# Optimization experiments

Hardware: AMD Instinct MI355X
Metric: run time of the kernel (lower is better)

The kernel has to match this reference:

```python
import jax, jax.numpy as jnp
import numpy as np

T, D, H, E = 8192, 1024, 512, 8
BLK = 32  # MXFP8 scaling block size along the contraction dim


def setup_inputs() -> dict:
    key = jax.random.key(0)
    k1, k2, k3, k4 = jax.random.split(key, 4)
    # qdata: values representable-ish in e4m3 (we use small normal floats)
    output_e4m3 = jax.random.normal(k1, (T, D), dtype=jnp.float32)
    # e8m0 scales are powers of two, one per 32-element block along dim
    output_scales_e8m0 = jnp.exp2(
        jax.random.randint(k2, (T, D // BLK), -2, 3).astype(jnp.float32)
    )
    # uniform token distribution across experts (tokens are expert-contiguous)
    num_tokens_per_expert = jnp.full((E,), T // E, dtype=jnp.int32)
    expert_padded_offsets = jnp.zeros((E,), dtype=jnp.int32)  # unused by forward body
    w13 = jax.random.normal(k3, (E, 2 * H, D), dtype=jnp.float32) * 0.02
    w2 = jax.random.normal(k4, (E, D, H), dtype=jnp.float32) * 0.02
    return {
        "output_e4m3": output_e4m3,
        "output_scales_e8m0": output_scales_e8m0,
        "num_tokens_per_expert": num_tokens_per_expert,
        "expert_padded_offsets": expert_padded_offsets,
        "w13": w13,
        "w2": w2,
    }


def reference(output_e4m3, output_scales_e8m0, num_tokens_per_expert,
              expert_padded_offsets, w13, w2):
    # Dequantize MXFP8: qdata * per-block e8m0 scale, blocks of 32 along dim.
    scales = jnp.repeat(output_scales_e8m0, BLK, axis=-1)  # [T, D]
    x = output_e4m3 * scales  # [T, D] high-precision reference activations
    # Grouped GEMM 1: tokens are expert-contiguous with uniform group sizes,
    # so the ragged grouped matmul reduces to a batched einsum per expert.
    tpe = T // E
    xg = x.reshape(E, tpe, D)                       # [E, tpe, D]
    h13 = jnp.einsum("etd,ehd->eth", xg, w13)       # [E, tpe, 2H]
    h1, h3 = h13[..., :H], h13[..., H:]
    h = jax.nn.silu(h1) * h3                        # fused SiLU-gate
    # Grouped GEMM 2
    out = jnp.einsum("eth,edh->etd", h, w2)         # [E, tpe, D]
    return out.reshape(T, D)
```

## Files before the change

kernel.cpp:

```cpp
#include <hip/hip_runtime.h>
#include <hip/hip_bf16.h>

#define T_TOK 8192
#define DDIM  1024
#define HDIM  512
#define NE    8
#define TPE   (T_TOK / NE)

typedef __attribute__((ext_vector_type(4))) float floatx4;
typedef __attribute__((ext_vector_type(8))) short bf16x8;

#define SBAR() __builtin_amdgcn_sched_barrier(0)

__device__ __forceinline__ unsigned short f2bf(float f) {
    union { float f; unsigned int u; } v;
    v.f = f;
    unsigned int u = v.u;
    unsigned int r = u + 0x7FFFu + ((u >> 16) & 1u);
    return (unsigned short)(r >> 16);
}

__device__ __forceinline__ unsigned int cvt_pk_bf16(float lo, float hi) {
    unsigned int r;
    asm("v_cvt_pk_bf16_f32 %0, %1, %2" : "=v"(r) : "v"(lo), "v"(hi));
    return r;
}

__device__ __forceinline__ void gld_lds16(const void* g, void* l) {
    __builtin_amdgcn_global_load_lds(
        (const __attribute__((address_space(1))) unsigned int*)g,
        (__attribute__((address_space(3))) unsigned int*)l, 16, 0, 0);
}

__global__ __launch_bounds__(256)
void convert_x_kernel(const float* __restrict__ X, const float* __restrict__ S,
                      unsigned short* __restrict__ Xb)
{
    const int NTX = (T_TOK * DDIM) / 4;
    const int stride = gridDim.x * blockDim.x;
    for (int i = blockIdx.x * blockDim.x + threadIdx.x; i < NTX; i += stride) {
        int row = i >> 8;
        int c4  = i & 255;
        float4 v = reinterpret_cast<const float4*>(X)[i];
        float sc = S[row * (DDIM / 32) + (c4 >> 3)];
        ushort4 b;
        b.x = f2bf(v.x * sc); b.y = f2bf(v.y * sc);
        b.z = f2bf(v.z * sc); b.w = f2bf(v.w * sc);
        reinterpret_cast<ushort4*>(Xb)[i] = b;
    }
}

__device__ __forceinline__ int xcd_swizzle_512(int raw) {
    return (raw & 7) * 64 + (raw >> 3);
}


__global__ __launch_bounds__(256, 2)
void gemm1_silu_kernel(const unsigned short* __restrict__ Xb,
                       const float* __restrict__ W13,
                       __hip_bfloat16* __restrict__ Hout)
{
    const int bid = xcd_swizzle_512(blockIdx.x);
    const int e  = bid >> 6;
    const int mt = (bid >> 3) & 7;
    const int nt = bid & 7;
    const int tok0 = e * TPE + mt * 128;
    const float* __restrict__ We = W13 + (size_t)e * (2 * HDIM) * DDIM;

    __shared__ __hip_bfloat16 sA[2][128][64];
    __shared__ __hip_bfloat16 sB[2][128][64];

    const int tid  = threadIdx.x;
    const int lane = tid & 63;
    const int wave = tid >> 6;
    const int wr = wave >> 1;
    const int wc = wave & 1;
    const int lr = lane & 15;
    const int sw0 = ((lane >> 4) ^ (lane & 7));

    floatx4 acc1[4][2] = {};
    floatx4 acc3[4][2] = {};

    const int srow0 = (tid >> 3);
    const int c8    = (tid & 7) * 8;
    const int dcol  = (tid & 7) * 8;
    const int gcol  = ((tid & 7) ^ (srow0 & 7)) * 8;
    const int swcol = gcol;

    float4 rB0[8], rB1[8];

    auto LOADB = [&](int kk, float4* rB) {
        const int k0 = kk * 64;
        #pragma unroll
        for (int j = 0; j < 4; ++j) {
            int row = srow0 + j * 32;
            int wrow = (j < 2) ? (nt * 64 + row)
                               : (HDIM + nt * 64 + (row - 64));
            const float* p = &We[(size_t)wrow * DDIM + k0 + c8];
            rB[2*j]   = *reinterpret_cast<const float4*>(p);
            rB[2*j+1] = *reinterpret_cast<const float4*>(p + 4);
        }
    };
    auto STAGEA = [&](int kk, int buf) {
        const int k0 = kk * 64;
        #pragma unroll
        for (int j = 0; j < 4; ++j) {
            int row = srow0 + j * 32;
            gld_lds16(&Xb[(size_t)(tok0 + row) * DDIM + k0 + gcol],
                      &sA[buf][row][dcol]);
        }
    };
    auto WRITEB = [&](int buf, const float4* rB) {
        #pragma unroll
        for (int j = 0; j < 4; ++j) {
            int row = srow0 + j * 32;
            uint4 w;
            w.x = cvt_pk_bf16(rB[2*j].x,   rB[2*j].y);
            w.y = cvt_pk_bf16(rB[2*j].z,   rB[2*j].w);
            w.z = cvt_pk_bf16(rB[2*j+1].x, rB[2*j+1].y);
            w.w = cvt_pk_bf16(rB[2*j+1].z, rB[2*j+1].w);
            *reinterpret_cast<uint4*>(&sB[buf][row][swcol]) = w;
        }
    };
    auto COMPUTE_KS = [&](int buf, int ks) {
        const int rc = (sw0 ^ (ks << 2)) << 3;
        bf16x8 a[4], b1[2], b3[2];
        #pragma unroll
        for (int m = 0; m < 4; ++m)
            a[m] = *reinterpret_cast<const bf16x8*>(&sA[buf][wr * 64 + m * 16 + lr][rc]);
        #pragma unroll
        for (int n = 0; n < 2; ++n) {
            b1[n] = *reinterpret_cast<const bf16x8*>(&sB[buf][wc * 32 + n * 16 + lr][rc]);
            b3[n] = *reinterpret_cast<const bf16x8*>(&sB[buf][64 + wc * 32 + n * 16 + lr][rc]);
        }
        #pragma unroll
        for (int m = 0; m < 4; ++m)
            #pragma unroll
            for (int n = 0; n < 2; ++n) {
                acc1[m][n] = __builtin_amdgcn_mfma_f32_16x16x32_bf16(a[m], b1[n], acc1[m][n], 0, 0, 0);
                acc3[m][n] = __builtin_amdgcn_mfma_f32_16x16x32_bf16(a[m], b3[n], acc3[m][n], 0, 0, 0);
            }
    };

    LOADB(0, rB0);  SBAR();
    STAGEA(0, 0);   SBAR();
    LOADB(1, rB1);  SBAR();
    asm volatile("s_waitcnt vmcnt(12)" ::: "memory");
    SBAR();
    WRITEB(0, rB0); SBAR();
    asm volatile("s_waitcnt vmcnt(8) lgkmcnt(0)" ::: "memory");
    SBAR();
    __builtin_amdgcn_s_barrier();

    for (int t = 0; t < DDIM / 64 - 2; t += 2) {
        STAGEA(t + 1, 1);   SBAR();
        LOADB(t + 2, rB0);  SBAR();
        COMPUTE_KS(0, 0);
        COMPUTE_KS(0, 1);
        asm volatile("s_waitcnt vmcnt(12)" ::: "memory");
        SBAR();
        WRITEB(1, rB1);     SBAR();
        asm volatile("s_waitcnt vmcnt(8) lgkmcnt(0)" ::: "memory");
        SBAR();
        __builtin_amdgcn_s_barrier();
        STAGEA(t + 2, 0);   SBAR();
        LOADB(t + 3, rB1);  SBAR();
        COMPUTE_KS(1, 0);
        COMPUTE_KS(1, 1);
        asm volatile("s_waitcnt vmcnt(12)" ::: "memory");
        SBAR();
        WRITEB(0, rB0);     SBAR();
        asm volatile("s_waitcnt vmcnt(8) lgkmcnt(0)" ::: "memory");
        SBAR();
        __builtin_amdgcn_s_barrier();
    }

    STAGEA(15, 1);    SBAR();
    COMPUTE_KS(0, 0);
    COMPUTE_KS(0, 1);
    asm volatile("s_waitcnt vmcnt(4)" ::: "memory");
    SBAR();
    WRITEB(1, rB1);   SBAR();
    asm volatile("s_waitcnt vmcnt(0) lgkmcnt(0)" ::: "memory");
    SBAR();
    __builtin_amdgcn_s_barrier();
    COMPUTE_KS(1, 0);
    COMPUTE_KS(1, 1);

    const int hcol0 = nt * 64 + wc * 32;
    #pragma unroll
    for (int m = 0; m < 4; ++m) {
        #pragma unroll
        for (int n = 0; n < 2; ++n) {
            #pragma unroll
            for (int i = 0; i < 4; ++i) {
                int row = tok0 + wr * 64 + m * 16 + (lane >> 4) * 4 + i;
                int col = hcol0 + n * 16 + (lane & 15);
                float h1 = acc1[m][n][i];
                float h3 = acc3[m][n][i];
                float sig = 1.0f / (1.0f + __expf(-h1));
                Hout[(size_t)row * HDIM + col] = __float2bfloat16(h1 * sig * h3);
            }
        }
    }
}

__global__ __launch_bounds__(256, 2)
void gemm2_kernel(const __hip_bfloat16* __restrict__ Hin,
                  const float* __restrict__ W2,
                  float* __restrict__ Out)
{
    const int bid = xcd_swizzle_512(blockIdx.x);
    const int e  = bid >> 6;
    const int nt = (bid >> 3) & 7;
    const int mt = bid & 7;
    const int tok0 = e * TPE + mt * 128;
    const float* __restrict__ We = W2 + (size_t)e * DDIM * HDIM;

    __shared__ __hip_bfloat16 sA[2][128][64];
    __shared__ __hip_bfloat16 sB[2][128][64];

    const int tid  = threadIdx.x;
    const int lane = tid & 63;
    const int wave = tid >> 6;
    const int wr = wave >> 1;
    const int wc = wave & 1;
    const int lr = lane & 15;
    const int sw0 = ((lane >> 4) ^ (lane & 7));

    floatx4 acc[4][4] = {};

    const int srow0 = (tid >> 3);
    const int c8    = (tid & 7) * 8;
    const int dcol  = (tid & 7) * 8;
    const int swcol = ((tid & 7) ^ (srow0 & 7)) * 8;

    float4 rB0[8], rB1[8];

    auto LOADB = [&](int kk, float4* rB) {
        const int k0 = kk * 64;
        #pragma unroll
        for (int j = 0; j < 4; ++j) {
            int row = srow0 + j * 32;
            const float* p = &We[(size_t)(nt * 128 + row) * HDIM + k0 + c8];
            rB[2*j]   = *reinterpret_cast<const float4*>(p);
            rB[2*j+1] = *reinterpret_cast<const float4*>(p + 4);
        }
    };
    auto STAGEA = [&](int kk, int buf) {
        const int k0 = kk * 64;
        #pragma unroll
        for (int j = 0; j < 4; ++j) {
            int row = srow0 + j * 32;
            gld_lds16(&Hin[(size_t)(tok0 + row) * HDIM + k0 + swcol],
                      &sA[buf][row][dcol]);
        }
    };
    auto WRITEB = [&](int buf, const float4* rB) {
        #pragma unroll
        for (int j = 0; j < 4; ++j) {
            int row = srow0 + j * 32;
            uint4 w;
            w.x = cvt_pk_bf16(rB[2*j].x,   rB[2*j].y);
            w.y = cvt_pk_bf16(rB[2*j].z,   rB[2*j].w);
            w.z = cvt_pk_bf16(rB[2*j+1].x, rB[2*j+1].y);
            w.w = cvt_pk_bf16(rB[2*j+1].z, rB[2*j+1].w);
            *reinterpret_cast<uint4*>(&sB[buf][row][swcol]) = w;
        }
    };
    auto COMPUTE = [&](int buf) {
        #pragma unroll
        for (int ks = 0; ks < 2; ++ks) {
            const int rc = (sw0 ^ (ks << 2)) << 3;
            bf16x8 a[4], b[4];
            #pragma unroll
            for (int m = 0; m < 4; ++m)
                a[m] = *reinterpret_cast<const bf16x8*>(&sA[buf][wr * 64 + m * 16 + lr][rc]);
            #pragma unroll
            for (int n = 0; n < 4; ++n)
                b[n] = *reinterpret_cast<const bf16x8*>(&sB[buf][wc * 64 + n * 16 + lr][rc]);
            #pragma unroll
            for (int m = 0; m < 4; ++m)
                #pragma unroll
                for (int n = 0; n < 4; ++n)
                    acc[m][n] = __builtin_amdgcn_mfma_f32_16x16x32_bf16(a[m], b[n], acc[m][n], 0, 0, 0);
        }
    };

    LOADB(0, rB0);  SBAR();
    STAGEA(0, 0);   SBAR();
    LOADB(1, rB1);  SBAR();
    asm volatile("s_waitcnt vmcnt(12)" ::: "memory");
    SBAR();
    WRITEB(0, rB0); SBAR();
    asm volatile("s_waitcnt vmcnt(8) lgkmcnt(0)" ::: "memory");
    SBAR();
    __builtin_amdgcn_s_barrier();

    for (int t = 0; t < HDIM / 64 - 2; t += 2) {
        STAGEA(t + 1, 1);   SBAR();
        LOADB(t + 2, rB0);  SBAR();
        COMPUTE(0);
        asm volatile("s_waitcnt vmcnt(12)" ::: "memory");
        SBAR();
        WRITEB(1, rB1);     SBAR();
        asm volatile("s_waitcnt vmcnt(8) lgkmcnt(0)" ::: "memory");
        SBAR();
        __builtin_amdgcn_s_barrier();
        STAGEA(t + 2, 0);   SBAR();
        LOADB(t + 3, rB1);  SBAR();
        COMPUTE(1);
        asm volatile("s_waitcnt vmcnt(12)" ::: "memory");
        SBAR();
        WRITEB(0, rB0);     SBAR();
        asm volatile("s_waitcnt vmcnt(8) lgkmcnt(0)" ::: "memory");
        SBAR();
        __builtin_amdgcn_s_barrier();
    }

    STAGEA(7, 1);   SBAR();
    COMPUTE(0);
    asm volatile("s_waitcnt vmcnt(4)" ::: "memory");
    SBAR();
    WRITEB(1, rB1); SBAR();
    asm volatile("s_waitcnt vmcnt(0) lgkmcnt(0)" ::: "memory");
    SBAR();
    __builtin_amdgcn_s_barrier();
    COMPUTE(1);

    const int dcol0 = nt * 128 + wc * 64;
    #pragma unroll
    for (int m = 0; m < 4; ++m) {
        #pragma unroll
        for (int n = 0; n < 4; ++n) {
            #pragma unroll
            for (int i = 0; i < 4; ++i) {
                int row = tok0 + wr * 64 + m * 16 + (lane >> 4) * 4 + i;
                int col = dcol0 + n * 16 + (lane & 15);
                Out[(size_t)row * DDIM + col] = acc[m][n][i];
            }
        }
    }
}

extern "C" void kernel_launch(void* const* d_in, const int* in_sizes, int n_in,
                              void* d_out, int out_size, void* d_ws, size_t ws_size,
                              hipStream_t stream) {
    const float* X   = (const float*)d_in[0];
    const float* S   = (const float*)d_in[1];
    const float* W13 = (const float*)d_in[4];
    const float* W2  = (const float*)d_in[5];
    float* Out = (float*)d_out;

    __hip_bfloat16* Hb = (__hip_bfloat16*)d_ws;
    unsigned short* Xb = (unsigned short*)d_out;

    convert_x_kernel<<<2048, 256, 0, stream>>>(X, S, Xb);
    gemm1_silu_kernel<<<NE * 8 * 8, 256, 0, stream>>>(Xb, W13, Hb);
    gemm2_kernel<<<NE * 8 * 8, 256, 0, stream>>>(Hb, W2, Out);
}
```

Measured before the change: 55.91 us.

## Enlarge gemm1 M-tile to 256 rows with 512-thread blocks

The GEMM1+SiLU kernel now computes a 256-token by 128-column tile with 8 waves instead of a 128x128 tile with 4 waves, halving the grid to 256 blocks. Each fp32 W13 tile is converted to bf16 and reused across twice as many tokens, cutting redundant weight reads and conversions. B staging is redistributed so each thread loads one float4 per row, with a new swizzled LDS write and adjusted vmcnt waits. The cost is larger LDS use per block and one block per CU, which reduces latency hiding.

```diff
diff --git a/kernel.cpp b/kernel.cpp
--- a/kernel.cpp
+++ b/kernel.cpp
@@ -53,21 +53,24 @@
 __device__ __forceinline__ int xcd_swizzle_512(int raw) {
     return (raw & 7) * 64 + (raw >> 3);
 }
-
-
-__global__ __launch_bounds__(256, 2)
+__device__ __forceinline__ int xcd_swizzle_256(int raw) {
+    return (raw & 7) * 32 + (raw >> 3);
+}
+
+
+__global__ __launch_bounds__(512, 2)
 void gemm1_silu_kernel(const unsigned short* __restrict__ Xb,
                        const float* __restrict__ W13,
                        __hip_bfloat16* __restrict__ Hout)
 {
-    const int bid = xcd_swizzle_512(blockIdx.x);
-    const int e  = bid >> 6;
-    const int mt = (bid >> 3) & 7;
+    const int bid = xcd_swizzle_256(blockIdx.x);
+    const int e  = bid >> 5;
+    const int mt = (bid >> 3) & 3;
     const int nt = bid & 7;
-    const int tok0 = e * TPE + mt * 128;
+    const int tok0 = e * TPE + mt * 256;
     const float* __restrict__ We = W13 + (size_t)e * (2 * HDIM) * DDIM;
 
-    __shared__ __hip_bfloat16 sA[2][128][64];
+    __shared__ __hip_bfloat16 sA[2][256][64];
     __shared__ __hip_bfloat16 sB[2][128][64];
 
     const int tid  = threadIdx.x;
@@ -81,45 +84,45 @@
     floatx4 acc1[4][2] = {};
     floatx4 acc3[4][2] = {};
 
-    const int srow0 = (tid >> 3);
-    const int c8    = (tid & 7) * 8;
-    const int dcol  = (tid & 7) * 8;
-    const int gcol  = ((tid & 7) ^ (srow0 & 7)) * 8;
-    const int swcol = gcol;
-
-    float4 rB0[8], rB1[8];
+    const int srowA = tid >> 3;
+    const int dcolA = (tid & 7) * 8;
+    const int gcolA = ((tid & 7) ^ (srowA & 7)) * 8;
+    const int srowB = tid >> 4;
+    const int f4    = tid & 15;
+    const int bcol  = f4 * 4;
+
+    float4 rB0[4], rB1[4];
 
     auto LOADB = [&](int kk, float4* rB) {
         const int k0 = kk * 64;
         #pragma unroll
         for (int j = 0; j < 4; ++j) {
-            int row = srow0 + j * 32;
+            int row = srowB + j * 32;
             int wrow = (j < 2) ? (nt * 64 + row)
                                : (HDIM + nt * 64 + (row - 64));
-            const float* p = &We[(size_t)wrow * DDIM + k0 + c8];
-            rB[2*j]   = *reinterpret_cast<const float4*>(p);
-            rB[2*j+1] = *reinterpret_cast<const float4*>(p + 4);
+            rB[j] = *reinterpret_cast<const float4*>(
+                        &We[(size_t)wrow * DDIM + k0 + bcol]);
         }
     };
     auto STAGEA = [&](int kk, int buf) {
         const int k0 = kk * 64;
         #pragma unroll
         for (int j = 0; j < 4; ++j) {
-            int row = srow0 + j * 32;
-            gld_lds16(&Xb[(size_t)(tok0 + row) * DDIM + k0 + gcol],
-                      &sA[buf][row][dcol]);
+            int row = srowA + j * 64;
+            gld_lds16(&Xb[(size_t)(tok0 + row) * DDIM + k0 + gcolA],
+                      &sA[buf][row][dcolA]);
         }
     };
     auto WRITEB = [&](int buf, const float4* rB) {
         #pragma unroll
         for (int j = 0; j < 4; ++j) {
-            int row = srow0 + j * 32;
-            uint4 w;
-            w.x = cvt_pk_bf16(rB[2*j].x,   rB[2*j].y);
-            w.y = cvt_pk_bf16(rB[2*j].z,   rB[2*j].w);
-            w.z = cvt_pk_bf16(rB[2*j+1].x, rB[2*j+1].y);
-            w.w = cvt_pk_bf16(rB[2*j+1].z, rB[2*j+1].w);
-            *reinterpret_cast<uint4*>(&sB[buf][row][swcol]) = w;
+            int row = srowB + j * 32;
+            uint2 w;
+            w.x = cvt_pk_bf16(rB[j].x, rB[j].y);
+            w.y = cvt_pk_bf16(rB[j].z, rB[j].w);
+            char* base = reinterpret_cast<char*>(&sB[buf][row][0]);
+            int off = (((f4 >> 1) ^ (row & 7)) << 4) + ((f4 & 1) << 3);
+            *reinterpret_cast<uint2*>(base + off) = w;
         }
     };
     auto COMPUTE_KS = [&](int buf, int ks) {
@@ -145,10 +148,10 @@
     LOADB(0, rB0);  SBAR();
     STAGEA(0, 0);   SBAR();
     LOADB(1, rB1);  SBAR();
-    asm volatile("s_waitcnt vmcnt(12)" ::: "memory");
+    asm volatile("s_waitcnt vmcnt(8)" ::: "memory");
     SBAR();
     WRITEB(0, rB0); SBAR();
-    asm volatile("s_waitcnt vmcnt(8) lgkmcnt(0)" ::: "memory");
+    asm volatile("s_waitcnt vmcnt(4) lgkmcnt(0)" ::: "memory");
     SBAR();
     __builtin_amdgcn_s_barrier();
 
@@ -157,20 +160,20 @@
         LOADB(t + 2, rB0);  SBAR();
         COMPUTE_KS(0, 0);
         COMPUTE_KS(0, 1);
-        asm volatile("s_waitcnt vmcnt(12)" ::: "memory");
+        asm volatile("s_waitcnt vmcnt(8)" ::: "memory");
         SBAR();
         WRITEB(1, rB1);     SBAR();
-        asm volatile("s_waitcnt vmcnt(8) lgkmcnt(0)" ::: "memory");
+        asm volatile("s_waitcnt vmcnt(4) lgkmcnt(0)" ::: "memory");
         SBAR();
         __builtin_amdgcn_s_barrier();
         STAGEA(t + 2, 0);   SBAR();
         LOADB(t + 3, rB1);  SBAR();
         COMPUTE_KS(1, 0);
         COMPUTE_KS(1, 1);
-        asm volatile("s_waitcnt vmcnt(12)" ::: "memory");
+        asm volatile("s_waitcnt vmcnt(8)" ::: "memory");
         SBAR();
         WRITEB(0, rB0);     SBAR();
-        asm volatile("s_waitcnt vmcnt(8) lgkmcnt(0)" ::: "memory");
+        asm volatile("s_waitcnt vmcnt(4) lgkmcnt(0)" ::: "memory");
         SBAR();
         __builtin_amdgcn_s_barrier();
     }
@@ -356,6 +359,6 @@
     unsigned short* Xb = (unsigned short*)d_out;
 
     convert_x_kernel<<<2048, 256, 0, stream>>>(X, S, Xb);
-    gemm1_silu_kernel<<<NE * 8 * 8, 256, 0, stream>>>(Xb, W13, Hb);
+    gemm1_silu_kernel<<<NE * 4 * 8, 512, 0, stream>>>(Xb, W13, Hb);
     gemm2_kernel<<<NE * 8 * 8, 256, 0, stream>>>(Hb, W2, Out);
 }
```

Result: faster. 54.49 us, median of 2 (-2.5%).
